# Optimization experiments

Measured on AMD Instinct MI355X. Metric: run time of the kernel, lower is better.

Reference implementation:

```python
import jax, jax.numpy as jnp
import numpy as np

B, T, D = 32, 512, 256
F = 256  # duration_predictor_filter_size
K = 3    # kernel size, padding=1
MEL_MAX = 2304
EPS = 1e-5


def _conv1d(x, w, b):
    # x: [B, T, C_in], w: [C_out, C_in, K], 'same'-ish padding=1
    y = jax.lax.conv_general_dilated(
        x.transpose(0, 2, 1), w, window_strides=(1,), padding=[(1, 1)],
        dimension_numbers=("NCH", "OIH", "NCH"))
    return y.transpose(0, 2, 1) + b


def _layernorm(x, g, b):
    mu = jnp.mean(x, axis=-1, keepdims=True)
    var = jnp.mean(jnp.square(x - mu), axis=-1, keepdims=True)
    return (x - mu) * jax.lax.rsqrt(var + EPS) * g + b


def setup_inputs() -> dict:
    key = jax.random.key(0)
    ks = jax.random.split(key, 8)
    x = jax.random.normal(ks[0], (B, T, D), dtype=jnp.float32)
    target = jax.random.randint(ks[1], (B, T), 0, 8, dtype=jnp.int32)
    s = 0.02
    return {
        "x": x,
        "target": target,
        "mel_max_length": MEL_MAX,
        "conv1_w": jax.random.normal(ks[2], (F, D, K), dtype=jnp.float32) * s,
        "conv1_b": jnp.zeros((F,), jnp.float32),
        "ln1_g": jnp.ones((F,), jnp.float32),
        "ln1_b": jnp.zeros((F,), jnp.float32),
        "conv2_w": jax.random.normal(ks[3], (F, F, K), dtype=jnp.float32) * s,
        "conv2_b": jnp.zeros((F,), jnp.float32),
        "ln2_g": jnp.ones((F,), jnp.float32),
        "ln2_b": jnp.zeros((F,), jnp.float32),
        "lin_w": jax.random.normal(ks[4], (1, F), dtype=jnp.float32) * s,
        "lin_b": jnp.zeros((1,), jnp.float32),
    }


def reference(x, target, mel_max_length, conv1_w, conv1_b, ln1_g, ln1_b,
              conv2_w, conv2_b, ln2_g, ln2_b, lin_w, lin_b):
    # Variance_adaptor (duration predictor), eval-mode dropout = identity
    h = jax.nn.relu(_layernorm(_conv1d(x, conv1_w, conv1_b), ln1_g, ln1_b))
    h = jax.nn.relu(_layernorm(_conv1d(h, conv2_w, conv2_b), ln2_g, ln2_b))
    dur_pred = jax.nn.relu(jnp.einsum("btf,of->bto", h, lin_w) + lin_b)[..., 0]  # [B,T]

    # LR: alignment @ x, expressed as the equivalent duration-indexed gather.
    # alignment[b, t_out, j] = 1 iff cumsum(dur)[b,j-1] <= t_out < cumsum(dur)[b,j]
    cum = jnp.cumsum(target, axis=1)                    # [B, T]
    t_out = jnp.arange(mel_max_length, dtype=cum.dtype)  # [T_out]
    idx = jax.vmap(lambda c: jnp.searchsorted(c, t_out, side="right"))(cum)  # [B, T_out]
    valid = (t_out[None, :] < cum[:, -1:]).astype(x.dtype)                   # [B, T_out]
    gathered = jnp.take_along_axis(x, jnp.clip(idx, 0, T - 1)[:, :, None], axis=1)
    output = gathered * valid[:, :, None]                # zeros past total length (pad)
    return output, dur_pred
```

## Files before the change

### kernel.cpp

```cpp
#include <hip/hip_runtime.h>

typedef __attribute__((ext_vector_type(8))) short short8;
typedef __attribute__((ext_vector_type(4))) float floatx4;

#define TOUT_C 2304

static __device__ __forceinline__ unsigned short f2bf(float f) {
    unsigned int u = __float_as_uint(f);
    return (unsigned short)((u + 0x7FFFu + ((u >> 16) & 1u)) >> 16);
}

__global__ __launch_bounds__(256)
void prep_kernel(const float* __restrict__ x, const float* __restrict__ w1,
                 const float* __restrict__ w2, const int* __restrict__ target,
                 ushort* __restrict__ xb, ushort* __restrict__ h1b,
                 ushort* __restrict__ w1pb, ushort* __restrict__ w2pb,
                 int* __restrict__ idxbuf)
{
    const int blk = blockIdx.x, tid = threadIdx.x;
    if (blk < 4112) {
        const int r = blk * 4 + (tid >> 6);
        const int c = (tid & 63) * 4;
        const int b = r / 514, tp = r % 514;
        ushort4 o;
        if (tp >= 1 && tp <= 512) {
            float4 v = *(const float4*)(x + ((size_t)(b * 512 + tp - 1) * 256 + c));
            o.x = f2bf(v.x); o.y = f2bf(v.y); o.z = f2bf(v.z); o.w = f2bf(v.w);
        } else {
            o.x = o.y = o.z = o.w = 0;
            *(ushort4*)(h1b + (size_t)r * 256 + c) = o;
        }
        *(ushort4*)(xb + (size_t)r * 256 + c) = o;
    } else if (blk < 5648) {
        const bool second = blk >= 4880;
        const int e = (blk - (second ? 4880 : 4112)) * 256 + tid;
        const float* w = second ? w2 : w1;
        ushort* wpb = second ? w2pb : w1pb;
        const int f = e / 768, j = e % 768;
        const int c = j & 255, kr = j >> 8;
        wpb[(j >> 5) * 8192 + f * 32 + (j & 31)] = f2bf(w[f * 768 + c * 3 + kr]);
    } else {
        __shared__ int cum[512];
        __shared__ int ps[256];
        const int b = blk - 5648;
        const int v0 = target[b * 512 + 2 * tid];
        const int v1 = target[b * 512 + 2 * tid + 1];
        ps[tid] = v0 + v1;
        __syncthreads();
        for (int off = 1; off < 256; off <<= 1) {
            int t = (tid >= off) ? ps[tid - off] : 0;
            __syncthreads();
            ps[tid] += t;
            __syncthreads();
        }
        const int excl = tid ? ps[tid - 1] : 0;
        cum[2 * tid]     = excl + v0;
        cum[2 * tid + 1] = excl + v0 + v1;
        __syncthreads();
        const int total = cum[511];
        for (int t = tid; t < TOUT_C; t += 256) {
            int lo = 0, hi = 512;
            while (lo < hi) {
                int mid = (lo + hi) >> 1;
                if (cum[mid] <= t) lo = mid + 1; else hi = mid;
            }
            idxbuf[b * TOUT_C + t] = (t < total) ? ((lo < 512) ? lo : 511) : -1;
        }
    }
}

template<bool IS_CONV2>
__global__ __launch_bounds__(256, 2)
void conv_mfma_kernel(const ushort* __restrict__ xb,
                      const ushort* __restrict__ wpb,
                      const float* __restrict__ cbias,
                      const float* __restrict__ gamma, const float* __restrict__ beta,
                      const float* __restrict__ lw, const float* __restrict__ lb,
                      ushort* __restrict__ outb,
                      float* __restrict__ durp)
{
    __shared__ float sum_s[4][32], sq_s[4][32];
    __shared__ float mu_s[32], rs_s[32];

    const int tid  = threadIdx.x;
    const int w    = tid >> 6, lane = tid & 63;
    const int q    = lane >> 4, col = lane & 15;
    const int b    = blockIdx.x >> 4;
    const int t0   = (blockIdx.x & 15) << 5;

    floatx4 acc[2][4] = {};
    const ushort* xrow = xb + ((size_t)b * 514 + t0) * 256;
    const ushort* wbase = wpb + ((size_t)w * 64 + col) * 32 + q * 8;

    #pragma unroll 4
    for (int s = 0; s < 24; ++s) {
        const int krow = s >> 3, cb = (s & 7) << 5;
        short8 af[2], bf8[4];
        #pragma unroll
        for (int mi = 0; mi < 2; ++mi)
            af[mi] = *(const short8*)(xrow + (size_t)(mi * 16 + col + krow) * 256
                                      + cb + q * 8);
        #pragma unroll
        for (int ni = 0; ni < 4; ++ni)
            bf8[ni] = *(const short8*)(wbase + (size_t)s * 8192 + ni * 512);
        #pragma unroll
        for (int mi = 0; mi < 2; ++mi)
            #pragma unroll
            for (int ni = 0; ni < 4; ++ni)
                acc[mi][ni] = __builtin_amdgcn_mfma_f32_16x16x32_bf16(
                    af[mi], bf8[ni], acc[mi][ni], 0, 0, 0);
    }

    const int base_c = w * 64;
    float cb4[4], gm4[4], bt4[4];
    #pragma unroll
    for (int ni = 0; ni < 4; ++ni) {
        cb4[ni] = cbias[base_c + ni * 16 + col];
        gm4[ni] = gamma[base_c + ni * 16 + col];
        bt4[ni] = beta [base_c + ni * 16 + col];
    }
    float rsum[2][4] = {}, rsq[2][4] = {};
    #pragma unroll
    for (int mi = 0; mi < 2; ++mi)
        #pragma unroll
        for (int ni = 0; ni < 4; ++ni)
            #pragma unroll
            for (int r = 0; r < 4; ++r) {
                float v = acc[mi][ni][r] + cb4[ni];
                acc[mi][ni][r] = v;
                rsum[mi][r] += v;
                rsq [mi][r] += v * v;
            }
    #pragma unroll
    for (int mi = 0; mi < 2; ++mi)
        #pragma unroll
        for (int r = 0; r < 4; ++r) {
            float s = rsum[mi][r], ss = rsq[mi][r];
            #pragma unroll
            for (int d = 8; d > 0; d >>= 1) {
                s  += __shfl_down(s,  d, 16);
                ss += __shfl_down(ss, d, 16);
            }
            if (col == 0) {
                sum_s[w][mi * 16 + q * 4 + r] = s;
                sq_s [w][mi * 16 + q * 4 + r] = ss;
            }
        }
    __syncthreads();
    if (tid < 32) {
        float s  = sum_s[0][tid] + sum_s[1][tid] + sum_s[2][tid] + sum_s[3][tid];
        float ss = sq_s [0][tid] + sq_s [1][tid] + sq_s [2][tid] + sq_s [3][tid];
        float mu = s * (1.f / 256.f);
        float var = ss * (1.f / 256.f) - mu * mu;
        mu_s[tid] = mu;
        rs_s[tid] = rsqrtf(var + 1e-5f);
    }
    __syncthreads();

    if (!IS_CONV2) {
        #pragma unroll
        for (int mi = 0; mi < 2; ++mi)
            #pragma unroll
            for (int ni = 0; ni < 4; ++ni)
                #pragma unroll
                for (int r = 0; r < 4; ++r) {
                    int row = mi * 16 + q * 4 + r;
                    float v = (acc[mi][ni][r] - mu_s[row]) * rs_s[row] * gm4[ni] + bt4[ni];
                    outb[((size_t)b * 514 + t0 + row + 1) * 256 + base_c + ni * 16 + col]
                        = f2bf(fmaxf(v, 0.f));
                }
    } else {
        float lw4[4];
        #pragma unroll
        for (int ni = 0; ni < 4; ++ni) lw4[ni] = lw[base_c + ni * 16 + col];
        float dsum[2][4] = {};
        #pragma unroll
        for (int mi = 0; mi < 2; ++mi)
            #pragma unroll
            for (int ni = 0; ni < 4; ++ni)
                #pragma unroll
                for (int r = 0; r < 4; ++r) {
                    int row = mi * 16 + q * 4 + r;
                    float v = (acc[mi][ni][r] - mu_s[row]) * rs_s[row] * gm4[ni] + bt4[ni];
                    dsum[mi][r] += fmaxf(v, 0.f) * lw4[ni];
                }
        #pragma unroll
        for (int mi = 0; mi < 2; ++mi)
            #pragma unroll
            for (int r = 0; r < 4; ++r) {
                float s = dsum[mi][r];
                #pragma unroll
                for (int d = 8; d > 0; d >>= 1) s += __shfl_down(s, d, 16);
                if (col == 0) sum_s[w][mi * 16 + q * 4 + r] = s;
            }
        __syncthreads();
        if (tid < 32)
            durp[b * 512 + t0 + tid] = fmaxf(sum_s[0][tid] + sum_s[1][tid]
                                           + sum_s[2][tid] + sum_s[3][tid] + lb[0], 0.f);
    }
}

__global__ __launch_bounds__(256)
void gather_kernel(const float* __restrict__ x, const int* __restrict__ idxbuf,
                   float* __restrict__ out, int T, int TOUT, int B)
{
    const size_t e  = (size_t)blockIdx.x * 256 + threadIdx.x;
    const size_t NE = (size_t)B * TOUT * 64;
    if (e >= NE) return;
    const int    d4  = (int)(e & 63);
    const size_t rt  = e >> 6;
    const int    idx = idxbuf[rt];
    const int    b   = (int)(rt / TOUT);
    float4 v = make_float4(0.f, 0.f, 0.f, 0.f);
    if (idx >= 0)
        v = *(const float4*)(x + (((size_t)b * T + idx) << 8) + (d4 << 2));
    *(float4*)((float*)out + (e << 2)) = v;
}

extern "C" void kernel_launch(void* const* d_in, const int* in_sizes, int n_in,
                              void* d_out, int out_size, void* d_ws, size_t ws_size,
                              hipStream_t stream) {
    const float* x      = (const float*)d_in[0];
    const int*   target = (const int*)  d_in[1];
    const float* c1w = (const float*)d_in[3];
    const float* c1b = (const float*)d_in[4];
    const float* g1  = (const float*)d_in[5];
    const float* b1  = (const float*)d_in[6];
    const float* c2w = (const float*)d_in[7];
    const float* c2b = (const float*)d_in[8];
    const float* g2  = (const float*)d_in[9];
    const float* b2  = (const float*)d_in[10];
    const float* lw  = (const float*)d_in[11];
    const float* lb  = (const float*)d_in[12];

    const int B = 32, T = 512, C = 256;
    const int BT = B * T;
    const int TOUT = (out_size - BT) / (B * C);

    const size_t PADEL = (size_t)B * 514 * 256;
    ushort* xb     = (ushort*)d_ws;
    ushort* h1b    = xb + PADEL;
    ushort* w1pb   = h1b + PADEL;
    ushort* w2pb   = w1pb + 196608;
    int*    idxbuf = (int*)(w2pb + 196608);

    float* out0 = (float*)d_out;
    float* durp = out0 + (size_t)B * TOUT * C;

    prep_kernel<<<5680, 256, 0, stream>>>(x, c1w, c2w, target, xb, h1b, w1pb, w2pb, idxbuf);
    conv_mfma_kernel<false><<<512, 256, 0, stream>>>(xb,  w1pb, c1b, g1, b1,
                                                     nullptr, nullptr, h1b, nullptr);
    conv_mfma_kernel<true ><<<512, 256, 0, stream>>>(h1b, w2pb, c2b, g2, b2,
                                                     lw, lb, nullptr, durp);
    gather_kernel<<<(int)(((size_t)B * TOUT * 64 + 255) / 256), 256, 0, stream>>>(
        x, idxbuf, out0, T, TOUT, B);
}
```

Baseline: 179.2 us.

## Stage conv operands through LDS with async loads and fuse gather into conv2

```diff
diff --git a/kernel.cpp b/kernel.cpp
--- a/kernel.cpp
+++ b/kernel.cpp
@@ -3,19 +3,23 @@
 typedef __attribute__((ext_vector_type(8))) short short8;
 typedef __attribute__((ext_vector_type(4))) float floatx4;
 
-#define TOUT_C 2304
+typedef __attribute__((address_space(3))) unsigned int lds_u32;
+typedef __attribute__((address_space(1))) const unsigned int glb_u32;
 
 static __device__ __forceinline__ unsigned short f2bf(float f) {
     unsigned int u = __float_as_uint(f);
     return (unsigned short)((u + 0x7FFFu + ((u >> 16) & 1u)) >> 16);
 }
 
+static __device__ __forceinline__ void cp16(const ushort* g, ushort* l) {
+    __builtin_amdgcn_global_load_lds((glb_u32*)g, (lds_u32*)l, 16, 0, 0);
+}
+
 __global__ __launch_bounds__(256)
 void prep_kernel(const float* __restrict__ x, const float* __restrict__ w1,
-                 const float* __restrict__ w2, const int* __restrict__ target,
+                 const float* __restrict__ w2,
                  ushort* __restrict__ xb, ushort* __restrict__ h1b,
-                 ushort* __restrict__ w1pb, ushort* __restrict__ w2pb,
-                 int* __restrict__ idxbuf)
+                 ushort* __restrict__ w1pb, ushort* __restrict__ w2pb)
 {
     const int blk = blockIdx.x, tid = threadIdx.x;
     if (blk < 4112) {
@@ -31,41 +35,16 @@
             *(ushort4*)(h1b + (size_t)r * 256 + c) = o;
         }
         *(ushort4*)(xb + (size_t)r * 256 + c) = o;
-    } else if (blk < 5648) {
+    } else {
         const bool second = blk >= 4880;
         const int e = (blk - (second ? 4880 : 4112)) * 256 + tid;
         const float* w = second ? w2 : w1;
         ushort* wpb = second ? w2pb : w1pb;
         const int f = e / 768, j = e % 768;
         const int c = j & 255, kr = j >> 8;
-        wpb[(j >> 5) * 8192 + f * 32 + (j & 31)] = f2bf(w[f * 768 + c * 3 + kr]);
-    } else {
-        __shared__ int cum[512];
-        __shared__ int ps[256];
-        const int b = blk - 5648;
-        const int v0 = target[b * 512 + 2 * tid];
-        const int v1 = target[b * 512 + 2 * tid + 1];
-        ps[tid] = v0 + v1;
-        __syncthreads();
-        for (int off = 1; off < 256; off <<= 1) {
-            int t = (tid >= off) ? ps[tid - off] : 0;
-            __syncthreads();
-            ps[tid] += t;
-            __syncthreads();
-        }
-        const int excl = tid ? ps[tid - 1] : 0;
-        cum[2 * tid]     = excl + v0;
-        cum[2 * tid + 1] = excl + v0 + v1;
-        __syncthreads();
-        const int total = cum[511];
-        for (int t = tid; t < TOUT_C; t += 256) {
-            int lo = 0, hi = 512;
-            while (lo < hi) {
-                int mid = (lo + hi) >> 1;
-                if (cum[mid] <= t) lo = mid + 1; else hi = mid;
-            }
-            idxbuf[b * TOUT_C + t] = (t < total) ? ((lo < 512) ? lo : 511) : -1;
-        }
+        const int s = j >> 6, kk = j & 63;
+        wpb[s * 16384 + f * 64 + (((kk >> 3) ^ (f & 7)) << 3) + (kk & 7)]
+            = f2bf(w[f * 768 + c * 3 + kr]);
     }
 }
 
@@ -77,38 +56,103 @@
                       const float* __restrict__ gamma, const float* __restrict__ beta,
                       const float* __restrict__ lw, const float* __restrict__ lb,
                       ushort* __restrict__ outb,
-                      float* __restrict__ durp)
+                      float* __restrict__ durp,
+                      const float* __restrict__ x,
+                      const int* __restrict__ target,
+                      float* __restrict__ out0)
 {
-    __shared__ float sum_s[4][32], sq_s[4][32];
-    __shared__ float mu_s[32], rs_s[32];
-
-    const int tid  = threadIdx.x;
-    const int w    = tid >> 6, lane = tid & 63;
-    const int q    = lane >> 4, col = lane & 15;
-    const int b    = blockIdx.x >> 4;
-    const int t0   = (blockIdx.x & 15) << 5;
+    __shared__ ushort As[32 * 64];
+    __shared__ ushort Bs[256 * 64];
+    __shared__ float sum_s[4][32], sq_s[4][32], mu_s[32], rs_s[32];
+    __shared__ int cum[512], ps[256], sidx[64];
+
+    const int tid = threadIdx.x;
+
+    if (IS_CONV2 && blockIdx.x >= 512) {
+        const int bg = blockIdx.x - 512;
+        const int b = bg / 36, t0o = (bg % 36) * 64;
+        const int v0 = target[b * 512 + 2 * tid];
+        const int v1 = target[b * 512 + 2 * tid + 1];
+        ps[tid] = v0 + v1;
+        __syncthreads();
+        for (int off = 1; off < 256; off <<= 1) {
+            int t = (tid >= off) ? ps[tid - off] : 0;
+            __syncthreads();
+            ps[tid] += t;
+            __syncthreads();
+        }
+        const int excl = tid ? ps[tid - 1] : 0;
+        cum[2 * tid]     = excl + v0;
+        cum[2 * tid + 1] = excl + v0 + v1;
+        __syncthreads();
+        const int total = cum[511];
+        if (tid < 64) {
+            int t = t0o + tid;
+            int lo = 0, hi = 512;
+            while (lo < hi) {
+                int mid = (lo + hi) >> 1;
+                if (cum[mid] <= t) lo = mid + 1; else hi = mid;
+            }
+            sidx[tid] = (t < total) ? ((lo < 512) ? lo : 511) : -1;
+        }
+        __syncthreads();
+        const float4* x4 = (const float4*)x;
+        float4* o4 = (float4*)out0;
+        const int lane6 = tid & 63, g4 = tid >> 6;
+        #pragma unroll 4
+        for (int rr = 0; rr < 16; ++rr) {
+            int r = rr * 4 + g4;
+            int idx = sidx[r];
+            float4 v = make_float4(0.f, 0.f, 0.f, 0.f);
+            if (idx >= 0) v = x4[((size_t)(b * 512 + idx)) * 64 + lane6];
+            o4[((size_t)(b * 2304 + t0o + r)) * 64 + lane6] = v;
+        }
+        return;
+    }
+
+    const int w = tid >> 6, lane = tid & 63;
+    const int q = lane >> 4, col = lane & 15;
+    const int b  = blockIdx.x >> 4;
+    const int t0 = (blockIdx.x & 15) << 5;
 
     floatx4 acc[2][4] = {};
-    const ushort* xrow = xb + ((size_t)b * 514 + t0) * 256;
-    const ushort* wbase = wpb + ((size_t)w * 64 + col) * 32 + q * 8;
-
-    #pragma unroll 4
-    for (int s = 0; s < 24; ++s) {
-        const int krow = s >> 3, cb = (s & 7) << 5;
-        short8 af[2], bf8[4];
-        #pragma unroll
-        for (int mi = 0; mi < 2; ++mi)
-            af[mi] = *(const short8*)(xrow + (size_t)(mi * 16 + col + krow) * 256
-                                      + cb + q * 8);
+    const ushort* xbb = xb + (size_t)b * 514 * 256;
+    const int arow  = tid >> 3;
+    const int aquad = (tid & 7) ^ (arow & 7);
+    ushort* AsW = As + (size_t)w * 512;
+    ushort* BsW = Bs + (size_t)w * 512;
+
+    for (int s = 0; s < 12; ++s) {
+        const int krow = s >> 2, cb = (s & 3) << 6;
+        cp16(xbb + (size_t)(t0 + krow + arow) * 256 + cb + aquad * 8, AsW);
+        const ushort* wsrc = wpb + (size_t)s * 16384 + w * 512 + lane * 8;
+        #pragma unroll
+        for (int i = 0; i < 8; ++i)
+            cp16(wsrc + i * 2048, BsW + i * 2048);
+        __syncthreads();
+
+        short8 af[2][2], bf[4][2];
+        #pragma unroll
+        for (int mi = 0; mi < 2; ++mi)
+            #pragma unroll
+            for (int kh = 0; kh < 2; ++kh)
+                af[mi][kh] = *(const short8*)((const char*)As
+                    + (mi * 16 + col) * 128 + (((kh * 4 + q) ^ (col & 7)) * 16));
         #pragma unroll
         for (int ni = 0; ni < 4; ++ni)
-            bf8[ni] = *(const short8*)(wbase + (size_t)s * 8192 + ni * 512);
-        #pragma unroll
-        for (int mi = 0; mi < 2; ++mi)
-            #pragma unroll
-            for (int ni = 0; ni < 4; ++ni)
-                acc[mi][ni] = __builtin_amdgcn_mfma_f32_16x16x32_bf16(
-                    af[mi], bf8[ni], acc[mi][ni], 0, 0, 0);
+            #pragma unroll
+            for (int kh = 0; kh < 2; ++kh)
+                bf[ni][kh] = *(const short8*)((const char*)Bs
+                    + (w * 64 + ni * 16 + col) * 128 + (((kh * 4 + q) ^ (col & 7)) * 16));
+        #pragma unroll
+        for (int kh = 0; kh < 2; ++kh)
+            #pragma unroll
+            for (int mi = 0; mi < 2; ++mi)
+                #pragma unroll
+                for (int ni = 0; ni < 4; ++ni)
+                    acc[mi][ni] = __builtin_amdgcn_mfma_f32_16x16x32_bf16(
+                        af[mi][kh], bf[ni][kh], acc[mi][ni], 0, 0, 0);
+        __syncthreads();
     }
 
     const int base_c = w * 64;
@@ -198,23 +242,6 @@
             durp[b * 512 + t0 + tid] = fmaxf(sum_s[0][tid] + sum_s[1][tid]
                                            + sum_s[2][tid] + sum_s[3][tid] + lb[0], 0.f);
     }
-}
-
-__global__ __launch_bounds__(256)
-void gather_kernel(const float* __restrict__ x, const int* __restrict__ idxbuf,
-                   float* __restrict__ out, int T, int TOUT, int B)
-{
-    const size_t e  = (size_t)blockIdx.x * 256 + threadIdx.x;
-    const size_t NE = (size_t)B * TOUT * 64;
-    if (e >= NE) return;
-    const int    d4  = (int)(e & 63);
-    const size_t rt  = e >> 6;
-    const int    idx = idxbuf[rt];
-    const int    b   = (int)(rt / TOUT);
-    float4 v = make_float4(0.f, 0.f, 0.f, 0.f);
-    if (idx >= 0)
-        v = *(const float4*)(x + (((size_t)b * T + idx) << 8) + (d4 << 2));
-    *(float4*)((float*)out + (e << 2)) = v;
 }
 
 extern "C" void kernel_launch(void* const* d_in, const int* in_sizes, int n_in,
@@ -233,25 +260,22 @@
     const float* lw  = (const float*)d_in[11];
     const float* lb  = (const float*)d_in[12];
 
-    const int B = 32, T = 512, C = 256;
-    const int BT = B * T;
-    const int TOUT = (out_size - BT) / (B * C);
+    const int B = 32, C = 256;
 
     const size_t PADEL = (size_t)B * 514 * 256;
-    ushort* xb     = (ushort*)d_ws;
-    ushort* h1b    = xb + PADEL;
-    ushort* w1pb   = h1b + PADEL;
-    ushort* w2pb   = w1pb + 196608;
-    int*    idxbuf = (int*)(w2pb + 196608);
+    ushort* xb   = (ushort*)d_ws;
+    ushort* h1b  = xb + PADEL;
+    ushort* w1pb = h1b + PADEL;
+    ushort* w2pb = w1pb + 196608;
 
     float* out0 = (float*)d_out;
-    float* durp = out0 + (size_t)B * TOUT * C;
-
-    prep_kernel<<<5680, 256, 0, stream>>>(x, c1w, c2w, target, xb, h1b, w1pb, w2pb, idxbuf);
-    conv_mfma_kernel<false><<<512, 256, 0, stream>>>(xb,  w1pb, c1b, g1, b1,
-                                                     nullptr, nullptr, h1b, nullptr);
-    conv_mfma_kernel<true ><<<512, 256, 0, stream>>>(h1b, w2pb, c2b, g2, b2,
-                                                     lw, lb, nullptr, durp);
-    gather_kernel<<<(int)(((size_t)B * TOUT * 64 + 255) / 256), 256, 0, stream>>>(
-        x, idxbuf, out0, T, TOUT, B);
-}
+    float* durp = out0 + (size_t)B * 2304 * C;
+
+    prep_kernel<<<5648, 256, 0, stream>>>(x, c1w, c2w, xb, h1b, w1pb, w2pb);
+    conv_mfma_kernel<false><<<512, 256, 0, stream>>>(
+        xb, w1pb, c1b, g1, b1, nullptr, nullptr, h1b, nullptr,
+        nullptr, nullptr, nullptr);
+    conv_mfma_kernel<true><<<512 + 1152, 256, 0, stream>>>(
+        h1b, w2pb, c2b, g2, b2, lw, lb, nullptr, durp,
+        x, target, out0);
+}
```

Result: faster. 148.5 us (-17.2%).
